# Optimization experiments

Measured on AMD Instinct MI355X. Metric: run time of the kernel, lower is better.

The kernel has to match this reference:

```python
import jax, jax.numpy as jnp
import numpy as np

B, S, HID = 1, 2048, 3072
NH, NKV, HD = 32, 8, 96
N_REP = NH // NKV
ROPE_THETA = 10000.0


def _rotate_half(x):
    half = x.shape[-1] // 2
    return jnp.concatenate([-x[..., half:], x[..., :half]], axis=-1)


def setup_inputs() -> dict:
    key = jax.random.key(0)
    k1, k2, k3 = jax.random.split(key, 3)
    hidden_states = jax.random.normal(k1, (B, S, HID), dtype=jnp.float32)
    qkv_w = jax.random.normal(k2, (NH * HD + 2 * NKV * HD, HID), dtype=jnp.float32) * 0.02
    o_w = jax.random.normal(k3, (HID, NH * HD), dtype=jnp.float32) * 0.02
    position_ids = jnp.broadcast_to(jnp.arange(S, dtype=jnp.int64)[None, :], (B, S))
    causal = jnp.tril(jnp.ones((S, S), dtype=bool))
    attention_mask = jnp.where(causal, 0.0, jnp.finfo(jnp.float32).min)[None, None].astype(jnp.float32)
    attention_mask = jnp.broadcast_to(attention_mask, (B, 1, S, S))
    return {"hidden_states": hidden_states, "position_ids": position_ids,
            "attention_mask": attention_mask, "qkv_w": qkv_w, "o_w": o_w}


def reference(hidden_states, position_ids, attention_mask, qkv_w, o_w):
    b, s, _ = hidden_states.shape
    qkv = jnp.einsum('bsh,oh->bso', hidden_states, qkv_w)
    q_pos = NH * HD
    q = qkv[..., :q_pos]
    k = qkv[..., q_pos:q_pos + NKV * HD]
    v = qkv[..., q_pos + NKV * HD:]
    # [b, heads, s, hd]
    q = q.reshape(b, s, NH, HD).transpose(0, 2, 1, 3)
    k = k.reshape(b, s, NKV, HD).transpose(0, 2, 1, 3)
    v = v.reshape(b, s, NKV, HD).transpose(0, 2, 1, 3)
    # RoPE
    inv_freq = 1.0 / (ROPE_THETA ** (jnp.arange(0, HD, 2, dtype=jnp.float32) / HD))
    freqs = position_ids.astype(jnp.float32)[:, :, None] * inv_freq[None, None, :]  # [b,s,hd/2]
    emb = jnp.concatenate([freqs, freqs], axis=-1)  # [b,s,hd]
    cos = jnp.cos(emb)[:, None, :, :]
    sin = jnp.sin(emb)[:, None, :, :]
    q = q * cos + _rotate_half(q) * sin
    k = k * cos + _rotate_half(k) * sin
    # GQA repeat_kv (repeat_interleave on head dim)
    k = jnp.repeat(k, N_REP, axis=1)
    v = jnp.repeat(v, N_REP, axis=1)
    scores = jnp.einsum('bhqd,bhkd->bhqk', q, k) / jnp.sqrt(jnp.float32(HD))
    scores = scores + attention_mask
    w = jax.nn.softmax(scores.astype(jnp.float32), axis=-1).astype(v.dtype)
    attn = jnp.einsum('bhqk,bhkd->bhqd', w, v)
    attn = attn.transpose(0, 2, 1, 3).reshape(b, s, NH * HD)
    out = jnp.einsum('bsf,of->bso', attn, o_w)
    return out
```

## Files before the change

### kernel.cpp

```cpp
#include <hip/hip_runtime.h>

#define S_LEN 2048
#define HID_DIM 3072
#define NH 32
#define NKV 8
#define HD 96
#define QKV_OUT 4608

typedef __attribute__((ext_vector_type(8))) short short8;
typedef __attribute__((ext_vector_type(4))) float floatx4;

__device__ __forceinline__ unsigned short f2b(float f) {
    unsigned int u = __float_as_uint(f);
    u = (u + 0x7FFFu + ((u >> 16) & 1u)) >> 16;
    return (unsigned short)u;
}
__device__ __forceinline__ float b2f(unsigned short h) {
    return __uint_as_float(((unsigned int)h) << 16);
}
__device__ __forceinline__ void async_ld16(const void* g, void* l) {
    __builtin_amdgcn_global_load_lds((const __attribute__((address_space(1))) void*)g,
                                     (__attribute__((address_space(3))) void*)l, 16, 0, 0);
}
__device__ __forceinline__ float fast_exp2(float x) {
#if __has_builtin(__builtin_amdgcn_exp2f)
    return __builtin_amdgcn_exp2f(x);
#else
    return exp2f(x);
#endif
}
__device__ __forceinline__ void store_out(float* C, size_t i, float v) { C[i] = v; }
__device__ __forceinline__ void store_out(unsigned short* C, size_t i, float v) { C[i] = f2b(v); }


__global__ void cvt3_tiled(const float* __restrict__ a, int nab,
                           const float* __restrict__ b, int nbb,
                           const float* __restrict__ c, int ncb,
                           unsigned short* __restrict__ oa,
                           unsigned short* __restrict__ ob,
                           unsigned short* __restrict__ oc) {
    int wid = blockIdx.x * 4 + (threadIdx.x >> 6);
    const int l = threadIdx.x & 63;
    const float* src;
    unsigned short* dst;
    int j = wid;
    if (j < nab) { src = a; dst = oa; }
    else {
        j -= nab;
        if (j < nbb) { src = b; dst = ob; }
        else {
            j -= nbb;
            if (j >= ncb) return;
            src = c; dst = oc;
        }
    }
    const int KB = HID_DIM >> 5;
    int rt = j / KB, kc = j - rt * KB;
    int i = l & 15, q = l >> 4;
    const float* p = src + ((size_t)rt * 16 + i) * HID_DIM + kc * 32 + q * 8;
    float4 v0 = *(const float4*)p;
    float4 v1 = *(const float4*)(p + 4);
    short8 o;
    o[0] = (short)f2b(v0.x); o[1] = (short)f2b(v0.y);
    o[2] = (short)f2b(v0.z); o[3] = (short)f2b(v0.w);
    o[4] = (short)f2b(v1.x); o[5] = (short)f2b(v1.y);
    o[6] = (short)f2b(v1.z); o[7] = (short)f2b(v1.w);
    *(short8*)(dst + (size_t)j * 512 + l * 8) = o;
}

template <typename OUT, int NBU, int WNU>
__global__ __launch_bounds__(256, 1) void gemm_pipe(const unsigned short* __restrict__ A,
                                                    const unsigned short* __restrict__ B,
                                                    OUT* __restrict__ C, int M, int N, int K) {
    extern __shared__ __attribute__((aligned(16))) char smem_raw[];
    unsigned short* lds = (unsigned short*)smem_raw;
    constexpr int NSLOT = 16 + 2 * NBU;
    constexpr int SLOTS = NSLOT / 4;
    constexpr int BUF = NSLOT * 512;
    static_assert(NSLOT % 4 == 0, "slot split");
    const int KB = K >> 5;
    const int NT = K >> 6;
    const int t = threadIdx.x, w = t >> 6, l = t & 63;
    const int lane15 = l & 15, quad = l >> 4;
    const int wm = (w >> 1) * 4;
    const int wn = (w & 1) * WNU;
    const int rowt0 = blockIdx.y * 8;
    const int colt0 = blockIdx.x * NBU;

    const floatx4 vzero = {0.f, 0.f, 0.f, 0.f};
    floatx4 acc[4][WNU];
#pragma unroll
    for (int i = 0; i < 4; ++i)
#pragma unroll
        for (int j = 0; j < WNU; ++j) acc[i][j] = vzero;

    const unsigned short* gsrc[SLOTS];
    int ldst[SLOTS];
#pragma unroll
    for (int j = 0; j < SLOTS; ++j) {
        int s = w * SLOTS + j;
        if (s < 16) {
            gsrc[j] = A + ((size_t)(rowt0 + (s >> 1)) * KB + (s & 1)) * 512 + l * 8;
        } else {
            int s2 = s - 16;
            gsrc[j] = B + ((size_t)(colt0 + (s2 >> 1)) * KB + (s2 & 1)) * 512 + l * 8;
        }
        ldst[j] = s * 512 + l * 8;
    }

#define STAGE(T)                                                             \
    {                                                                        \
        unsigned short* base_ = lds + (((T) & 1) ? BUF : 0);                 \
        size_t koff_ = (size_t)(T) * 1024;                                   \
        _Pragma("unroll")                                                    \
        for (int j = 0; j < SLOTS; ++j)                                      \
            async_ld16(gsrc[j] + koff_, base_ + ldst[j]);                    \
    }

    STAGE(0);
    for (int T = 0; T < NT; ++T) {
        if (T + 1 < NT) {
            STAGE(T + 1);
            if constexpr (SLOTS == 13)
                asm volatile("s_waitcnt vmcnt(13)" ::: "memory");
            else if constexpr (SLOTS == 10)
                asm volatile("s_waitcnt vmcnt(10)" ::: "memory");
            else
                asm volatile("s_waitcnt vmcnt(0)" ::: "memory");
        } else {
            asm volatile("s_waitcnt vmcnt(0)" ::: "memory");
        }
        __builtin_amdgcn_s_barrier();
        asm volatile("" ::: "memory");
        __builtin_amdgcn_s_setprio(1);

        const unsigned short* buf = lds + ((T & 1) ? BUF : 0);
#pragma unroll
        for (int kkb = 0; kkb < 2; ++kkb) {
            short8 af[4], bf[WNU];
#pragma unroll
            for (int mi = 0; mi < 4; ++mi)
                af[mi] = *(const short8*)(buf + ((wm + mi) * 2 + kkb) * 512 + l * 8);
#pragma unroll
            for (int ni = 0; ni < WNU; ++ni)
                bf[ni] = *(const short8*)(buf + (16 + (wn + ni) * 2 + kkb) * 512 + l * 8);
#pragma unroll
            for (int mi = 0; mi < 4; ++mi)
#pragma unroll
                for (int ni = 0; ni < WNU; ++ni)
                    acc[mi][ni] = __builtin_amdgcn_mfma_f32_16x16x32_bf16(af[mi], bf[ni], acc[mi][ni], 0, 0, 0);
        }

        __builtin_amdgcn_s_setprio(0);
        asm volatile("" ::: "memory");
        __builtin_amdgcn_s_barrier();
    }
#undef STAGE

#pragma unroll
    for (int mi = 0; mi < 4; ++mi)
#pragma unroll
        for (int ni = 0; ni < WNU; ++ni)
#pragma unroll
            for (int r = 0; r < 4; ++r) {
                int m = rowt0 * 16 + (w >> 1) * 64 + mi * 16 + quad * 4 + r;
                int n = colt0 * 16 + (w & 1) * (WNU * 16) + ni * 16 + lane15;
                store_out(C, (size_t)m * N + n, acc[mi][ni][r]);
            }
}

__global__ void rope_split(const unsigned short* __restrict__ qkv,
                           unsigned short* __restrict__ Qd,
                           unsigned short* __restrict__ Kd,
                           unsigned short* __restrict__ Vd) {
    const int s = blockIdx.x;
    const int t = threadIdx.x;
    const unsigned short* row = qkv + (size_t)s * QKV_OUT;
    const float L2T_48 = 0.2768273412406135f;
    const float SCALE2 = 0.14724444f;

    for (int i = t; i < NH * 48; i += 256) {
        int h = i / 48, d = i - (i / 48) * 48;
        float f = (float)s * exp2f(-(float)d * L2T_48);
        float sn, cs;
        sincosf(f, &sn, &cs);
        float q1 = b2f(row[h * 96 + d]);
        float q2 = b2f(row[h * 96 + d + 48]);
        size_t base = ((size_t)h * S_LEN + s) * HD;
        Qd[base + d] = f2b((q1 * cs - q2 * sn) * SCALE2);
        Qd[base + d + 48] = f2b((q2 * cs + q1 * sn) * SCALE2);
    }
    for (int i = t; i < NKV * 48; i += 256) {
        int h = i / 48, d = i - (i / 48) * 48;
        float f = (float)s * exp2f(-(float)d * L2T_48);
        float sn, cs;
        sincosf(f, &sn, &cs);
        float k1 = b2f(row[3072 + h * 96 + d]);
        float k2 = b2f(row[3072 + h * 96 + d + 48]);
        size_t base = ((size_t)h * S_LEN + s) * HD;
        Kd[base + d] = f2b(k1 * cs - k2 * sn);
        Kd[base + d + 48] = f2b(k2 * cs + k1 * sn);
    }
    for (int i = t; i < NKV * HD; i += 256) {
        int h = i / 96, d = i - (i / 96) * 96;
        Vd[((size_t)h * S_LEN + s) * HD + d] = row[3840 + i];
    }
}

__global__ void transpose_v(const unsigned short* __restrict__ V,
                            unsigned short* __restrict__ Vt) {
    __shared__ unsigned short T[96][72];
    const int kvh = blockIdx.x >> 5;
    const int s0 = (blockIdx.x & 31) * 64;
    const int t = threadIdx.x;
#pragma unroll
    for (int it = 0; it < 3; ++it) {
        int c = it * 256 + t;
        int r = c / 12, c8 = c - r * 12;
        short8 v = *(const short8*)(V + ((size_t)kvh * S_LEN + s0 + r) * HD + c8 * 8);
#pragma unroll
        for (int j = 0; j < 8; ++j) T[c8 * 8 + j][r] = (unsigned short)v[j];
    }
    __syncthreads();
#pragma unroll
    for (int it = 0; it < 3; ++it) {
        int c = it * 256 + t;
        int d = c >> 3, c8 = c & 7;
        short8 v;
#pragma unroll
        for (int j = 0; j < 8; ++j) v[j] = (short)T[d][c8 * 8 + j];
        *(short8*)(Vt + ((size_t)kvh * HD + d) * S_LEN + s0 + c8 * 8) = v;
    }
}

#define ATTN_M0 8.0f
__global__ __launch_bounds__(256) void attn_fwd(const unsigned short* __restrict__ Q,
                                                const unsigned short* __restrict__ K,
                                                const unsigned short* __restrict__ Vt,
                                                unsigned short* __restrict__ O) {
    __shared__ unsigned short Qs[4 * 3 * 512];
    __shared__ unsigned short Ks[12 * 512];
    __shared__ unsigned short Vs[12 * 512];
    __shared__ unsigned short Ps[4][16 * 72];
    const int h = blockIdx.x;
    const int qt = (int)gridDim.y - 1 - blockIdx.y;
    const int kvh = h >> 2;
    const int q0 = qt * 64;
    const int t = threadIdx.x, w = t >> 6, l = t & 63;
    const int lane15 = l & 15, quad = l >> 4;
    unsigned short* Pw = Ps[w];

    const unsigned short* Qg = Q + ((size_t)h * S_LEN + q0) * HD;
#pragma unroll
    for (int kkb = 0; kkb < 3; ++kkb)
        async_ld16(Qg + (w * 16 + lane15) * HD + kkb * 32 + quad * 8,
                   Qs + (w * 3 + kkb) * 512 + l * 8);

    int koff[3], voff0[3];
    long vofS[3];
#pragma unroll
    for (int j = 0; j < 3; ++j) {
        int c = w * 3 + j;
        int ct = c & 3, kkb = c >> 2;
        koff[j] = (ct * 16 + lane15) * HD + kkb * 32 + quad * 8;
        int nt = c % 6, kb2 = c / 6;
        vofS[j] = (long)(nt * 16 + lane15) * S_LEN + kb2 * 32 + quad * 8;
        voff0[j] = c * 512 + l * 8;
    }

    const floatx4 vzero = {0.f, 0.f, 0.f, 0.f};
    floatx4 accO[6];
#pragma unroll
    for (int nt = 0; nt < 6; ++nt) accO[nt] = vzero;
    float lsum[4] = {0.f, 0.f, 0.f, 0.f};

    const unsigned short* Kg = K + (size_t)kvh * S_LEN * HD;
    const unsigned short* Vg = Vt + (size_t)kvh * HD * S_LEN;
    const int qrow0 = q0 + w * 16 + quad * 4;

    for (int kt = 0; kt <= qt; ++kt) {
        const int k0 = kt * 64;
        __syncthreads();
#pragma unroll
        for (int j = 0; j < 3; ++j) {
            int c = w * 3 + j;
            async_ld16(Kg + (size_t)k0 * HD + koff[j], Ks + c * 512 + l * 8);
            async_ld16(Vg + k0 + vofS[j], Vs + voff0[j]);
        }
        __syncthreads();

        floatx4 accS[4];
#pragma unroll
        for (int ct = 0; ct < 4; ++ct) accS[ct] = vzero;
#pragma unroll
        for (int kkb = 0; kkb < 3; ++kkb) {
            short8 aq = *(const short8*)(Qs + (w * 3 + kkb) * 512 + l * 8);
#pragma unroll
            for (int ct = 0; ct < 4; ++ct) {
                short8 bk = *(const short8*)(Ks + (kkb * 4 + ct) * 512 + l * 8);
                accS[ct] = __builtin_amdgcn_mfma_f32_16x16x32_bf16(aq, bk, accS[ct], 0, 0, 0);
            }
        }

        if (kt < qt) {
#pragma unroll
            for (int ct = 0; ct < 4; ++ct)
#pragma unroll
                for (int r = 0; r < 4; ++r) {
                    float p = fast_exp2(accS[ct][r] - ATTN_M0);
                    lsum[r] += p;
                    Pw[(quad * 4 + r) * 72 + ct * 16 + lane15] = f2b(p);
                }
        } else {
#pragma unroll
            for (int ct = 0; ct < 4; ++ct) {
                int kcol = k0 + ct * 16 + lane15;
#pragma unroll
                for (int r = 0; r < 4; ++r) {
                    float s = (kcol <= qrow0 + r) ? accS[ct][r] - ATTN_M0 : -1.0e30f;
                    float p = fast_exp2(s);
                    lsum[r] += p;
                    Pw[(quad * 4 + r) * 72 + ct * 16 + lane15] = f2b(p);
                }
            }
        }

#pragma unroll
        for (int kb2 = 0; kb2 < 2; ++kb2) {
            short8 ap = *(const short8*)(Pw + lane15 * 72 + kb2 * 32 + quad * 8);
#pragma unroll
            for (int nt = 0; nt < 6; ++nt) {
                short8 bv = *(const short8*)(Vs + (kb2 * 6 + nt) * 512 + l * 8);
                accO[nt] = __builtin_amdgcn_mfma_f32_16x16x32_bf16(ap, bv, accO[nt], 0, 0, 0);
            }
        }
    }

    for (int off = 1; off < 16; off <<= 1)
#pragma unroll
        for (int r = 0; r < 4; ++r) lsum[r] += __shfl_xor(lsum[r], off, 64);
    float inv[4];
#pragma unroll
    for (int r = 0; r < 4; ++r) inv[r] = 1.f / lsum[r];
    const int srow0 = q0 + w * 16 + quad * 4;
#pragma unroll
    for (int nt = 0; nt < 6; ++nt) {
        int n = h * HD + nt * 16 + lane15;
        size_t base = ((size_t)(srow0 >> 4) * (HID_DIM >> 5) + (n >> 5)) * 512
                      + ((n & 31) >> 3) * 128 + (n & 7);
#pragma unroll
        for (int r = 0; r < 4; ++r) {
            int m15 = (srow0 + r) & 15;
            O[base + m15 * 8] = f2b(accO[nt][r] * inv[r]);
        }
    }
}

extern "C" void kernel_launch(void* const* d_in, const int* in_sizes, int n_in,
                              void* d_out, int out_size, void* d_ws, size_t ws_size,
                              hipStream_t stream) {
    const float* hidden = (const float*)d_in[0];
    const float* qkv_w = (const float*)d_in[3];
    const float* o_w = (const float*)d_in[4];
    float* out = (float*)d_out;

    unsigned short* Xb = (unsigned short*)d_ws;
    unsigned short* Wq = Xb + (size_t)S_LEN * HID_DIM;
    unsigned short* Wo = Wq + (size_t)QKV_OUT * HID_DIM;
    unsigned short* QKVb = Wo + (size_t)HID_DIM * HID_DIM;
    unsigned short* Qb = QKVb + (size_t)S_LEN * QKV_OUT;
    unsigned short* Kb = Qb + (size_t)NH * S_LEN * HD;
    unsigned short* Vb = Kb + (size_t)NKV * S_LEN * HD;
    unsigned short* Ab = Vb + (size_t)NKV * S_LEN * HD;
    unsigned short* Vtb = QKVb;

    static bool lds_init = false;
    if (!lds_init) {
        hipFuncSetAttribute(reinterpret_cast<const void*>(&gemm_pipe<unsigned short, 18, 9>),
                            hipFuncAttributeMaxDynamicSharedMemorySize, 106496);
        hipFuncSetAttribute(reinterpret_cast<const void*>(&gemm_pipe<float, 12, 6>),
                            hipFuncAttributeMaxDynamicSharedMemorySize, 81920);
        lds_init = true;
    }

    int nab = S_LEN * HID_DIM / 512, nbb = QKV_OUT * HID_DIM / 512, ncb = HID_DIM * HID_DIM / 512;
    int nblk = nab + nbb + ncb;
    cvt3_tiled<<<nblk / 4, 256, 0, stream>>>(hidden, nab, qkv_w, nbb, o_w, ncb, Xb, Wq, Wo);

    gemm_pipe<unsigned short, 18, 9><<<dim3(QKV_OUT / 288, S_LEN / 128), 256, 106496, stream>>>(
        Xb, Wq, QKVb, S_LEN, QKV_OUT, HID_DIM);
    rope_split<<<S_LEN, 256, 0, stream>>>(QKVb, Qb, Kb, Vb);
    transpose_v<<<NKV * (S_LEN / 64), 256, 0, stream>>>(Vb, Vtb);
    attn_fwd<<<dim3(NH, S_LEN / 64), 256, 0, stream>>>(Qb, Kb, Vtb, Ab);
    gemm_pipe<float, 12, 6><<<dim3(HID_DIM / 192, S_LEN / 128), 256, 81920, stream>>>(
        Ab, Wo, out, S_LEN, HID_DIM, HID_DIM);
}
```

Measured before the change: 334.1 us.

## Split-K the QKV GEMM into two partials and shrink the output GEMM tile

Adds a dedicated QKV GEMM that splits K in two across gridDim.z, writes bf16 partial results to two buffers, and uses a triple-buffered LDS pipeline. rope_split now sums the two partials before applying RoPE. The output projection GEMM switches to a smaller 6-column-tile configuration with two blocks per CU, and workspace buffers are reused. The goal is more blocks and better CU occupancy, at the cost of extra partial-buffer traffic and bf16 rounding of each partial before the sum.

```diff
diff --git a/kernel.cpp b/kernel.cpp
--- a/kernel.cpp
+++ b/kernel.cpp
@@ -68,8 +68,104 @@
     *(short8*)(dst + (size_t)j * 512 + l * 8) = o;
 }
 
+__global__ __launch_bounds__(256, 2) void gemm_qkv_sk(const unsigned short* __restrict__ A,
+                                                      const unsigned short* __restrict__ B,
+                                                      unsigned short* __restrict__ C0,
+                                                      unsigned short* __restrict__ C1) {
+    extern __shared__ __attribute__((aligned(16))) char smem_raw[];
+    unsigned short* lds = (unsigned short*)smem_raw;
+    const int KB = HID_DIM >> 5;
+    const int t = threadIdx.x, w = t >> 6, l = t & 63;
+    const int lane15 = l & 15, quad = l >> 4;
+    const int wm = (w >> 1) * 4;
+    const int wn = (w & 1) * 9;
+    const int rowt0 = blockIdx.y * 8;
+    const int colt0 = blockIdx.x * 18;
+    const int kc0 = blockIdx.z * 48;
+    unsigned short* __restrict__ C = blockIdx.z ? C1 : C0;
+
+    const floatx4 vzero = {0.f, 0.f, 0.f, 0.f};
+    floatx4 acc[4][9];
+#pragma unroll
+    for (int i = 0; i < 4; ++i)
+#pragma unroll
+        for (int j = 0; j < 9; ++j) acc[i][j] = vzero;
+
+    const int sbase = (w < 2) ? w * 7 : 14 + (w - 2) * 6;
+    const int scnt = (w < 2) ? 7 : 6;
+    const unsigned short* gsrc[7];
+    int ldst[7];
+#pragma unroll
+    for (int j = 0; j < 7; ++j) {
+        int s = sbase + (j < scnt ? j : scnt - 1);
+        if (s < 8) gsrc[j] = A + ((size_t)(rowt0 + s) * KB + kc0) * 512 + l * 8;
+        else       gsrc[j] = B + ((size_t)(colt0 + (s - 8)) * KB + kc0) * 512 + l * 8;
+        ldst[j] = s * 512 + l * 8;
+    }
+
+#define STAGE(TT, BIDX)                                                      \
+    {                                                                        \
+        unsigned short* b_ = lds + (BIDX) * (26 * 512);                      \
+        size_t ko_ = (size_t)(TT) * 512;                                     \
+        _Pragma("unroll")                                                    \
+        for (int j = 0; j < 7; ++j)                                          \
+            if (j < scnt) async_ld16(gsrc[j] + ko_, b_ + ldst[j]);           \
+    }
+#define VM2 { if (w < 2) asm volatile("s_waitcnt vmcnt(14)" ::: "memory");   \
+              else       asm volatile("s_waitcnt vmcnt(12)" ::: "memory"); }
+#define VM1 { if (w < 2) asm volatile("s_waitcnt vmcnt(7)" ::: "memory");    \
+              else       asm volatile("s_waitcnt vmcnt(6)" ::: "memory"); }
+#define COMPUTE(BIDX)                                                        \
+    {                                                                        \
+        const unsigned short* buf_ = lds + (BIDX) * (26 * 512);              \
+        short8 af[4], bfr[9];                                                \
+        _Pragma("unroll")                                                    \
+        for (int mi = 0; mi < 4; ++mi)                                       \
+            af[mi] = *(const short8*)(buf_ + (wm + mi) * 512 + l * 8);       \
+        _Pragma("unroll")                                                    \
+        for (int ni = 0; ni < 9; ++ni)                                       \
+            bfr[ni] = *(const short8*)(buf_ + (8 + wn + ni) * 512 + l * 8);  \
+        _Pragma("unroll")                                                    \
+        for (int mi = 0; mi < 4; ++mi)                                       \
+            _Pragma("unroll")                                                \
+            for (int ni = 0; ni < 9; ++ni)                                   \
+                acc[mi][ni] = __builtin_amdgcn_mfma_f32_16x16x32_bf16(af[mi], bfr[ni], acc[mi][ni], 0, 0, 0); \
+    }
+#define BAR  { asm volatile("" ::: "memory"); __builtin_amdgcn_s_barrier(); asm volatile("" ::: "memory"); }
+
+    STAGE(0, 0);
+    STAGE(1, 1);
+    for (int T = 0; T < 48; T += 3) {
+        STAGE(T + 2, 2); VM2; BAR;
+        __builtin_amdgcn_s_setprio(1); COMPUTE(0); __builtin_amdgcn_s_setprio(0); BAR;
+        if (T + 3 < 48) { STAGE(T + 3, 0); VM2; } else VM1;
+        BAR;
+        __builtin_amdgcn_s_setprio(1); COMPUTE(1); __builtin_amdgcn_s_setprio(0); BAR;
+        if (T + 4 < 48) { STAGE(T + 4, 1); VM2; }
+        else asm volatile("s_waitcnt vmcnt(0)" ::: "memory");
+        BAR;
+        __builtin_amdgcn_s_setprio(1); COMPUTE(2); __builtin_amdgcn_s_setprio(0); BAR;
+    }
+#undef STAGE
+#undef VM2
+#undef VM1
+#undef COMPUTE
+#undef BAR
+
+#pragma unroll
+    for (int mi = 0; mi < 4; ++mi)
+#pragma unroll
+        for (int ni = 0; ni < 9; ++ni)
+#pragma unroll
+            for (int r = 0; r < 4; ++r) {
+                int m = rowt0 * 16 + (w >> 1) * 64 + mi * 16 + quad * 4 + r;
+                int n = colt0 * 16 + (w & 1) * 144 + ni * 16 + lane15;
+                C[(size_t)m * QKV_OUT + n] = f2b(acc[mi][ni][r]);
+            }
+}
+
 template <typename OUT, int NBU, int WNU>
-__global__ __launch_bounds__(256, 1) void gemm_pipe(const unsigned short* __restrict__ A,
+__global__ __launch_bounds__(256, 2) void gemm_pipe(const unsigned short* __restrict__ A,
                                                     const unsigned short* __restrict__ B,
                                                     OUT* __restrict__ C, int M, int N, int K) {
     extern __shared__ __attribute__((aligned(16))) char smem_raw[];
@@ -125,6 +221,8 @@
                 asm volatile("s_waitcnt vmcnt(13)" ::: "memory");
             else if constexpr (SLOTS == 10)
                 asm volatile("s_waitcnt vmcnt(10)" ::: "memory");
+            else if constexpr (SLOTS == 7)
+                asm volatile("s_waitcnt vmcnt(7)" ::: "memory");
             else
                 asm volatile("s_waitcnt vmcnt(0)" ::: "memory");
         } else {
@@ -169,13 +267,15 @@
             }
 }
 
-__global__ void rope_split(const unsigned short* __restrict__ qkv,
+__global__ void rope_split(const unsigned short* __restrict__ p0,
+                           const unsigned short* __restrict__ p1,
                            unsigned short* __restrict__ Qd,
                            unsigned short* __restrict__ Kd,
                            unsigned short* __restrict__ Vd) {
     const int s = blockIdx.x;
     const int t = threadIdx.x;
-    const unsigned short* row = qkv + (size_t)s * QKV_OUT;
+    const unsigned short* r0 = p0 + (size_t)s * QKV_OUT;
+    const unsigned short* r1 = p1 + (size_t)s * QKV_OUT;
     const float L2T_48 = 0.2768273412406135f;
     const float SCALE2 = 0.14724444f;
 
@@ -184,8 +284,8 @@
         float f = (float)s * exp2f(-(float)d * L2T_48);
         float sn, cs;
         sincosf(f, &sn, &cs);
-        float q1 = b2f(row[h * 96 + d]);
-        float q2 = b2f(row[h * 96 + d + 48]);
+        float q1 = b2f(r0[h * 96 + d]) + b2f(r1[h * 96 + d]);
+        float q2 = b2f(r0[h * 96 + d + 48]) + b2f(r1[h * 96 + d + 48]);
         size_t base = ((size_t)h * S_LEN + s) * HD;
         Qd[base + d] = f2b((q1 * cs - q2 * sn) * SCALE2);
         Qd[base + d + 48] = f2b((q2 * cs + q1 * sn) * SCALE2);
@@ -195,15 +295,16 @@
         float f = (float)s * exp2f(-(float)d * L2T_48);
         float sn, cs;
         sincosf(f, &sn, &cs);
-        float k1 = b2f(row[3072 + h * 96 + d]);
-        float k2 = b2f(row[3072 + h * 96 + d + 48]);
+        float k1 = b2f(r0[3072 + h * 96 + d]) + b2f(r1[3072 + h * 96 + d]);
+        float k2 = b2f(r0[3072 + h * 96 + d + 48]) + b2f(r1[3072 + h * 96 + d + 48]);
         size_t base = ((size_t)h * S_LEN + s) * HD;
         Kd[base + d] = f2b(k1 * cs - k2 * sn);
         Kd[base + d + 48] = f2b(k2 * cs + k1 * sn);
     }
     for (int i = t; i < NKV * HD; i += 256) {
         int h = i / 96, d = i - (i / 96) * 96;
-        Vd[((size_t)h * S_LEN + s) * HD + d] = row[3840 + i];
+        Vd[((size_t)h * S_LEN + s) * HD + d] =
+            f2b(b2f(r0[3840 + i]) + b2f(r1[3840 + i]));
     }
 }
 
@@ -367,19 +468,18 @@
     unsigned short* Xb = (unsigned short*)d_ws;
     unsigned short* Wq = Xb + (size_t)S_LEN * HID_DIM;
     unsigned short* Wo = Wq + (size_t)QKV_OUT * HID_DIM;
-    unsigned short* QKVb = Wo + (size_t)HID_DIM * HID_DIM;
-    unsigned short* Qb = QKVb + (size_t)S_LEN * QKV_OUT;
-    unsigned short* Kb = Qb + (size_t)NH * S_LEN * HD;
-    unsigned short* Vb = Kb + (size_t)NKV * S_LEN * HD;
-    unsigned short* Ab = Vb + (size_t)NKV * S_LEN * HD;
-    unsigned short* Vtb = QKVb;
+    unsigned short* P0 = Wo + (size_t)HID_DIM * HID_DIM;
+    unsigned short* P1 = P0 + (size_t)S_LEN * QKV_OUT;
+    unsigned short* Ab = P1 + (size_t)S_LEN * QKV_OUT;
+    unsigned short* Qd = Xb;
+    unsigned short* Kd = Wq;
+    unsigned short* Vd = Wq + (size_t)NKV * S_LEN * HD;
+    unsigned short* Vtb = P0;
 
     static bool lds_init = false;
     if (!lds_init) {
-        hipFuncSetAttribute(reinterpret_cast<const void*>(&gemm_pipe<unsigned short, 18, 9>),
-                            hipFuncAttributeMaxDynamicSharedMemorySize, 106496);
-        hipFuncSetAttribute(reinterpret_cast<const void*>(&gemm_pipe<float, 12, 6>),
-                            hipFuncAttributeMaxDynamicSharedMemorySize, 81920);
+        hipFuncSetAttribute(reinterpret_cast<const void*>(&gemm_qkv_sk),
+                            hipFuncAttributeMaxDynamicSharedMemorySize, 79872);
         lds_init = true;
     }
 
@@ -387,11 +487,11 @@
     int nblk = nab + nbb + ncb;
     cvt3_tiled<<<nblk / 4, 256, 0, stream>>>(hidden, nab, qkv_w, nbb, o_w, ncb, Xb, Wq, Wo);
 
-    gemm_pipe<unsigned short, 18, 9><<<dim3(QKV_OUT / 288, S_LEN / 128), 256, 106496, stream>>>(
-        Xb, Wq, QKVb, S_LEN, QKV_OUT, HID_DIM);
-    rope_split<<<S_LEN, 256, 0, stream>>>(QKVb, Qb, Kb, Vb);
-    transpose_v<<<NKV * (S_LEN / 64), 256, 0, stream>>>(Vb, Vtb);
-    attn_fwd<<<dim3(NH, S_LEN / 64), 256, 0, stream>>>(Qb, Kb, Vtb, Ab);
-    gemm_pipe<float, 12, 6><<<dim3(HID_DIM / 192, S_LEN / 128), 256, 81920, stream>>>(
+    gemm_qkv_sk<<<dim3(QKV_OUT / 288, S_LEN / 128, 2), 256, 79872, stream>>>(
+        Xb, Wq, P0, P1);
+    rope_split<<<S_LEN, 256, 0, stream>>>(P0, P1, Qd, Kd, Vd);
+    transpose_v<<<NKV * (S_LEN / 64), 256, 0, stream>>>(Vd, Vtb);
+    attn_fwd<<<dim3(NH, S_LEN / 64), 256, 0, stream>>>(Qd, Kd, Vtb, Ab);
+    gemm_pipe<float, 6, 3><<<dim3(HID_DIM / 96, S_LEN / 128), 256, 57344, stream>>>(
         Ab, Wo, out, S_LEN, HID_DIM, HID_DIM);
 }
```

Measured after the change: 337.9 us. Within noise of the previous version (+1.1%).
